# Optimization experiments

Hardware: AMD Instinct MI355X
Metric: run time of the kernel (lower is better)

## Reference

```python
import jax, jax.numpy as jnp
import numpy as np

B = 32; IMG = 224; P = 16; D = 768; NH = 12; HD = 64; L = 12; MLP = 3072; S0 = 197
NE = 10; LP = 40; NPL = 5; NC = 100; EPS = 1e-6
POS_PROMPT = (0, 1, 2, 3, 4)


def setup_inputs() -> dict:
    ks = jax.random.split(jax.random.key(0), 18)
    n = lambda k, shp: jax.random.normal(k, shp, jnp.float32) * 0.02
    return {
        "inputs": jax.random.normal(ks[0], (B, 3, IMG, IMG), jnp.float32),
        "expert_ids": jax.random.randint(ks[1], (B,), 0, NE),
        "patch_w": n(ks[2], (D, 3, P, P)),
        "patch_b": n(ks[3], (D,)),
        "cls_token": n(ks[4], (1, 1, D)),
        "pos_embed": n(ks[5], (1, S0, D)),
        "ln1_s": jnp.ones((L, D), jnp.float32),
        "ln1_b": jnp.zeros((L, D), jnp.float32),
        "qkv_w": n(ks[6], (L, D, 3 * D)),
        "qkv_b": n(ks[7], (L, 3 * D)),
        "proj_w": n(ks[8], (L, D, D)),
        "proj_b": n(ks[9], (L, D)),
        "ln2_s": jnp.ones((L, D), jnp.float32),
        "ln2_b": jnp.zeros((L, D), jnp.float32),
        "fc1_w": n(ks[10], (L, D, MLP)),
        "fc1_b": n(ks[11], (L, MLP)),
        "fc2_w": n(ks[12], (L, MLP, D)),
        "fc2_b": n(ks[13], (L, D)),
        "norm_s": jnp.ones((D,), jnp.float32),
        "norm_b": jnp.zeros((D,), jnp.float32),
        "prompts": jax.random.uniform(ks[14], (NPL, NE, LP, D), jnp.float32),
        "head_w": n(ks[15], (NE, D, NC)),
        "head_b": n(ks[16], (NE, NC)),
    }


def _ln(x, s, b):
    m = x.mean(-1, keepdims=True)
    v = ((x - m) ** 2).mean(-1, keepdims=True)
    return (x - m) * jax.lax.rsqrt(v + EPS) * s + b


def _forward(inputs, expert_ids, patch_w, patch_b, cls_token, pos_embed,
             ln1_s, ln1_b, qkv_w, qkv_b, proj_w, proj_b, ln2_s, ln2_b,
             fc1_w, fc1_b, fc2_w, fc2_b, norm_s, norm_b, prompts, head_w, head_b):
    # patch embed: conv stride 16 -> [B, D, 14, 14] -> [B, 196, D]
    x = jax.lax.conv_general_dilated(inputs, patch_w, (P, P), 'VALID',
                                     dimension_numbers=('NCHW', 'OIHW', 'NCHW'))
    x = x.reshape(B, D, -1).transpose(0, 2, 1) + patch_b
    x = jnp.concatenate([jnp.broadcast_to(cls_token, (B, 1, D)), x], axis=1) + pos_embed
    # per-sample expert prompt gather: [B, NPL, LP, D], plus cls pos bias
    bp = jnp.take(prompts, expert_ids, axis=1).transpose(1, 0, 2, 3) + pos_embed[0, 0]
    scale = 1.0 / np.sqrt(HD)
    for i in range(L):
        if i in POS_PROMPT:
            x = jnp.concatenate([x, bp[:, POS_PROMPT.index(i)]], axis=1)
        S = x.shape[1]
        h = _ln(x, ln1_s[i], ln1_b[i])
        qkv = (h @ qkv_w[i] + qkv_b[i]).reshape(B, S, 3, NH, HD).transpose(2, 0, 3, 1, 4)
        q, k, v = qkv[0], qkv[1], qkv[2]
        att = jax.nn.softmax(jnp.einsum('bhqd,bhkd->bhqk', q, k) * scale, axis=-1)
        o = jnp.einsum('bhqk,bhkd->bhqd', att, v).transpose(0, 2, 1, 3).reshape(B, S, D)
        x = x + o @ proj_w[i] + proj_b[i]
        h = _ln(x, ln2_s[i], ln2_b[i])
        x = x + jax.nn.gelu(h @ fc1_w[i] + fc1_b[i], approximate=False) @ fc2_w[i] + fc2_b[i]
        x = x[:, :S0]  # drop prompt tokens after each block
    feat = _ln(x, norm_s, norm_b)[:, 0]
    # per-sample expert head dispatch: gathered-weight batched matvec
    return jnp.einsum('bd,bdc->bc', feat, head_w[expert_ids]) + head_b[expert_ids]


def reference(inputs, expert_ids, patch_w, patch_b, cls_token, pos_embed,
              ln1_s, ln1_b, qkv_w, qkv_b, proj_w, proj_b, ln2_s, ln2_b,
              fc1_w, fc1_b, fc2_w, fc2_b, norm_s, norm_b, prompts, head_w, head_b):
    return _forward(inputs, expert_ids, patch_w, patch_b, cls_token, pos_embed,
                    ln1_s, ln1_b, qkv_w, qkv_b, proj_w, proj_b, ln2_s, ln2_b,
                    fc1_w, fc1_b, fc2_w, fc2_b, norm_s, norm_b, prompts, head_w, head_b)
```

## Files before the change

### kernel.cpp

```cpp
#include <hip/hip_runtime.h>

typedef unsigned short ushort_t;
typedef __attribute__((ext_vector_type(8))) short short8;
typedef __attribute__((ext_vector_type(4))) float floatx4;

#define D_    768
#define SMAX  237
#define S0_   197
#define RPAD  7680
#define NHEAD 12
#define BATCH 32


__device__ __forceinline__ ushort_t f2bf(float f) {
  union { float f; unsigned u; } v; v.f = f;
  unsigned r = v.u + 0x7FFFu + ((v.u >> 16) & 1u);
  return (ushort_t)(r >> 16);
}
__device__ __forceinline__ float bf2f(ushort_t u) {
  union { unsigned u; float f; } v; v.u = ((unsigned)u) << 16; return v.f;
}
__device__ __forceinline__ void async16(const void* g, void* l) {
  __builtin_amdgcn_global_load_lds((const __attribute__((address_space(1))) void*)g,
                                   (__attribute__((address_space(3))) void*)l, 16, 0, 0);
}

__global__ __launch_bounds__(256) void patchify_kernel(
    const float* __restrict__ in, ushort_t* __restrict__ Xp) {
  int rowid = blockIdx.x;
  int b = rowid / 196, p = rowid - b * 196;
  int py = p / 14, px = p - py * 14;
  int tid = threadIdx.x;
#pragma unroll
  for (int t = 0; t < 3; ++t) {
    int k = tid + t * 256;
    int c = k >> 8, rem = k & 255, i = rem >> 4, j = rem & 15;
    float v = in[(((size_t)b * 3 + c) * 224 + py * 16 + i) * 224 + px * 16 + j];
    Xp[(size_t)rowid * 768 + k] = f2bf(v);
  }
}

__global__ void cvt_bf16_kernel(const float* __restrict__ src, ushort_t* __restrict__ dst, int n) {
  int i = blockIdx.x * 256 + threadIdx.x;
  if (i < n) dst[i] = f2bf(src[i]);
}

__global__ void cls_fill_kernel(const float* __restrict__ cls, const float* __restrict__ pos,
                                float* __restrict__ X) {
  int b = blockIdx.x, d = threadIdx.x;
  X[(size_t)b * 768 + d] = cls[d] + pos[d];
}

__global__ void prompt_fill_kernel(const float* __restrict__ prompts, const float* __restrict__ pos,
                                   const int* __restrict__ eid, float* __restrict__ X, int layer) {
  int id = blockIdx.x;
  int b = id / 40, p = id - b * 40;
  int e = eid[b];
  float v = prompts[(((size_t)layer * 10 + e) * 40 + p) * 768 + threadIdx.x] + pos[threadIdx.x];
  X[((size_t)(197 + p) * 32 + b) * 768 + threadIdx.x] = v;
}

__global__ __launch_bounds__(256) void transpose_wts_kernel(
    const float* __restrict__ qkvw, const float* __restrict__ projw,
    const float* __restrict__ fc1w, const float* __restrict__ fc2w,
    ushort_t* __restrict__ wq, ushort_t* __restrict__ wp,
    ushort_t* __restrict__ w1, ushort_t* __restrict__ w2) {
  int id = blockIdx.x;
  const float* src; ushort_t* dst; int K, N, t;
  if (id < 1728)      { src = qkvw; dst = wq; K = 768;  N = 2304; t = id; }
  else if (id < 2304) { src = projw; dst = wp; K = 768;  N = 768;  t = id - 1728; }
  else if (id < 4608) { src = fc1w; dst = w1; K = 768;  N = 3072; t = id - 2304; }
  else                { src = fc2w; dst = w2; K = 3072; N = 768;  t = id - 4608; }
  int ntn = N >> 5;
  int k0 = (t / ntn) * 32, n0 = (t % ntn) * 32;
  __shared__ float tile[32][33];
  int tx = threadIdx.x & 31, ty = threadIdx.x >> 5;
#pragma unroll
  for (int q = 0; q < 4; ++q) {
    int kk = q * 8 + ty;
    tile[kk][tx] = src[(size_t)(k0 + kk) * N + n0 + tx];
  }
  __syncthreads();
#pragma unroll
  for (int q = 0; q < 4; ++q) {
    int nn = q * 8 + ty;
    dst[(size_t)(n0 + nn) * K + k0 + tx] = f2bf(tile[tx][nn]);
  }
}

__global__ __launch_bounds__(256) void ln_kernel(
    const float* __restrict__ X, const float* __restrict__ s, const float* __restrict__ bt,
    ushort_t* __restrict__ H) {
  int row = blockIdx.x, tid = threadIdx.x;
  const float* xr = X + (size_t)row * 768;
  float v0 = xr[tid], v1 = xr[tid + 256], v2 = xr[tid + 512];
  float sum = v0 + v1 + v2;
  float sq = v0 * v0 + v1 * v1 + v2 * v2;
#pragma unroll
  for (int off = 32; off; off >>= 1) {
    sum += __shfl_down(sum, off, 64);
    sq  += __shfl_down(sq,  off, 64);
  }
  __shared__ float red[8];
  int wv = tid >> 6, ln = tid & 63;
  if (ln == 0) { red[wv] = sum; red[4 + wv] = sq; }
  __syncthreads();
  if (tid == 0) {
    red[0] = red[0] + red[1] + red[2] + red[3];
    red[4] = red[4] + red[5] + red[6] + red[7];
  }
  __syncthreads();
  float mean = red[0] * (1.f / 768.f);
  float var  = red[4] * (1.f / 768.f) - mean * mean;
  float rs = rsqrtf(var + 1e-6f);
  ushort_t* hr = H + (size_t)row * 768;
  hr[tid]       = f2bf((v0 - mean) * rs * s[tid]       + bt[tid]);
  hr[tid + 256] = f2bf((v1 - mean) * rs * s[tid + 256] + bt[tid + 256]);
  hr[tid + 512] = f2bf((v2 - mean) * rs * s[tid + 512] + bt[tid + 512]);
}

enum { EPI_BF16 = 0, EPI_GELU = 1, EPI_RESID = 2, EPI_PATCH = 3 };

template <int EPI>
__global__ __launch_bounds__(256) void gemm_kernel(
    const ushort_t* __restrict__ A, int lda,
    const ushort_t* __restrict__ BT, int ldb,
    const float* __restrict__ bias,
    float* __restrict__ XO, ushort_t* __restrict__ O,
    const float* __restrict__ pos,
    int N, int nx, int my, int Klen, int nt) {
  __shared__ ushort_t As[128 * 32];
  __shared__ ushort_t Bs[128 * 32];
  int per = gridDim.x >> 3;
  int F = blockIdx.x;
  int T = (F & 7) * per + (F >> 3);
  if (T >= nt) return;
  int n_i = T % nx, rest = T / nx;
  int m_i = rest % my, kz = rest / my;
  int m0 = m_i * 128, n0 = n_i * 128;
  int kb = kz * Klen, ke = kb + Klen;

  int tid = threadIdx.x, lane = tid & 63, wv = tid >> 6;
  int wm = (wv >> 1) * 64, wn = (wv & 1) * 64;
  int fr = lane & 15, kg = lane >> 4;
  int sw = (kg ^ ((fr >> 1) & 3)) * 8;

  floatx4 acc[4][4];
#pragma unroll
  for (int i = 0; i < 4; ++i)
#pragma unroll
    for (int j = 0; j < 4; ++j) acc[i][j] = (floatx4){0.f, 0.f, 0.f, 0.f};

  for (int k0 = kb; k0 < ke; k0 += 32) {
#pragma unroll
    for (int t = 0; t < 2; ++t) {
      int flat = (wv * 2 + t) * 64 + lane;
      int row = flat >> 2;
      int ch = ((flat & 3) ^ ((flat >> 3) & 3)) * 8;
      async16(A + (size_t)(m0 + row) * lda + k0 + ch, &As[(wv * 2 + t) * 512]);
      async16(BT + (size_t)(n0 + row) * ldb + k0 + ch, &Bs[(wv * 2 + t) * 512]);
    }
    __syncthreads();
    short8 af[4], bfr[4];
#pragma unroll
    for (int i = 0; i < 4; ++i) af[i] = *(const short8*)&As[(wm + i * 16 + fr) * 32 + sw];
#pragma unroll
    for (int j = 0; j < 4; ++j) bfr[j] = *(const short8*)&Bs[(wn + j * 16 + fr) * 32 + sw];
#pragma unroll
    for (int i = 0; i < 4; ++i)
#pragma unroll
      for (int j = 0; j < 4; ++j)
        acc[i][j] = __builtin_amdgcn_mfma_f32_16x16x32_bf16(af[i], bfr[j], acc[i][j], 0, 0, 0);
    __syncthreads();
  }

  int rbase = (lane >> 4) * 4;
#pragma unroll
  for (int i = 0; i < 4; ++i) {
#pragma unroll
    for (int j = 0; j < 4; ++j) {
      int col = n0 + wn + j * 16 + fr;
#pragma unroll
      for (int r = 0; r < 4; ++r) {
        int row = m0 + wm + i * 16 + rbase + r;
        if (EPI == EPI_BF16) {
          O[(size_t)row * N + col] = f2bf(acc[i][j][r] + bias[col]);
        } else if (EPI == EPI_GELU) {
          float v = acc[i][j][r] + bias[col];
          float g = 0.5f * v * (1.0f + erff(v * 0.70710678118f));
          O[(size_t)row * N + col] = f2bf(g);
        } else if (EPI == EPI_RESID) {
          float v = acc[i][j][r] + (kz == 0 ? bias[col] : 0.f);
          atomicAdd(&XO[(size_t)row * 768 + col], v);
        } else {
          int b = row / 196, p = row - b * 196;
          size_t orow = (size_t)(1 + p) * 32 + b;
          XO[orow * 768 + col] = acc[i][j][r] + bias[col] + pos[(size_t)(1 + p) * 768 + col];
        }
      }
    }
  }
}

__global__ __launch_bounds__(256) void attn_kernel(ushort_t* __restrict__ qkv, int S) {
  __shared__ ushort_t Kc[64 * 64];
  __shared__ ushort_t Vt[64 * 72];
  __shared__ ushort_t Pb[4][16 * 72];
  int id = blockIdx.x;
  int qc = id & 3, bh = id >> 2;
  int b = bh / NHEAD, h = bh - b * NHEAD;
  int tid = threadIdx.x, lane = tid & 63, wv = tid >> 6;
  int fr = lane & 15, kg = lane >> 4;
  int q0 = qc * 64 + wv * 16;

  int qr = q0 + fr; if (qr > S - 1) qr = S - 1;
  const ushort_t* qp = qkv + ((size_t)qr * 32 + b) * 2304 + h * 64 + kg * 8;
  short8 qf0 = *(const short8*)qp;
  short8 qf1 = *(const short8*)(qp + 32);

  floatx4 oacc[4];
#pragma unroll
  for (int j = 0; j < 4; ++j) oacc[j] = (floatx4){0.f, 0.f, 0.f, 0.f};
  float lsum[4] = {0.f, 0.f, 0.f, 0.f};

  int ksw = kg ^ (fr & 7);
  int kst_g = (lane & 7) ^ ((lane >> 3) & 7);

  for (int c = 0; c < 4; ++c) {
    int key0 = c * 64;
    __syncthreads();
#pragma unroll
    for (int t = 0; t < 2; ++t) {
      int f = (wv * 2 + t) * 64 + lane;
      int kr = key0 + (f >> 3); if (kr > S - 1) kr = S - 1;
      async16(qkv + ((size_t)kr * 32 + b) * 2304 + 768 + h * 64 + kst_g * 8,
              &Kc[(wv * 2 + t) * 512]);
    }
#pragma unroll
    for (int t = 0; t < 2; ++t) {
      int kc = wv * 2 + t;
      int vr = key0 + lane; if (vr > S - 1) vr = S - 1;
      short8 vv = *(const short8*)(qkv + ((size_t)vr * 32 + b) * 2304 + 1536 + h * 64 + kc * 8);
#pragma unroll
      for (int e = 0; e < 8; ++e) Vt[(kc * 8 + e) * 72 + lane] = (ushort_t)vv[e];
    }
    __syncthreads();

    floatx4 sacc[4];
#pragma unroll
    for (int j = 0; j < 4; ++j) sacc[j] = (floatx4){0.f, 0.f, 0.f, 0.f};
#pragma unroll
    for (int j = 0; j < 4; ++j) {
      int krow = j * 16 + fr;
      short8 b0 = *(const short8*)&Kc[krow * 64 + ksw * 8];
      short8 b1 = *(const short8*)&Kc[krow * 64 + (ksw ^ 4) * 8];
      sacc[j] = __builtin_amdgcn_mfma_f32_16x16x32_bf16(qf0, b0, sacc[j], 0, 0, 0);
      sacc[j] = __builtin_amdgcn_mfma_f32_16x16x32_bf16(qf1, b1, sacc[j], 0, 0, 0);
    }

#pragma unroll
    for (int j = 0; j < 4; ++j) {
      int key = key0 + j * 16 + fr;
      bool valid = key < S;
#pragma unroll
      for (int r = 0; r < 4; ++r) {
        float e = valid ? __expf(sacc[j][r] * 0.125f) : 0.f;
        lsum[r] += e;
        Pb[wv][(kg * 4 + r) * 72 + j * 16 + fr] = f2bf(e);
      }
    }
    __syncthreads();

    const ushort_t* pp = &Pb[wv][fr * 72 + kg * 8];
    short8 p0 = *(const short8*)pp;
    short8 p1 = *(const short8*)(pp + 32);
#pragma unroll
    for (int j = 0; j < 4; ++j) {
      const ushort_t* vp = &Vt[(j * 16 + fr) * 72 + kg * 8];
      short8 v0 = *(const short8*)vp;
      short8 v1 = *(const short8*)(vp + 32);
      oacc[j] = __builtin_amdgcn_mfma_f32_16x16x32_bf16(p0, v0, oacc[j], 0, 0, 0);
      oacc[j] = __builtin_amdgcn_mfma_f32_16x16x32_bf16(p1, v1, oacc[j], 0, 0, 0);
    }
  }

#pragma unroll
  for (int r = 0; r < 4; ++r) {
#pragma unroll
    for (int m = 1; m <= 8; m <<= 1) lsum[r] += __shfl_xor(lsum[r], m, 64);
  }
#pragma unroll
  for (int r = 0; r < 4; ++r) {
    int q = q0 + kg * 4 + r;
    if (q < S) {
      float inv = 1.f / lsum[r];
      ushort_t* op = qkv + ((size_t)q * 32 + b) * 2304 + h * 64;
#pragma unroll
      for (int j = 0; j < 4; ++j) op[j * 16 + fr] = f2bf(oacc[j][r] * inv);
    }
  }
}

__global__ __launch_bounds__(256) void head_kernel(
    const float* __restrict__ X, const float* __restrict__ ns, const float* __restrict__ nb,
    const int* __restrict__ eid, const float* __restrict__ hw, const float* __restrict__ hb,
    float* __restrict__ out) {
  int b = blockIdx.x, tid = threadIdx.x;
  const float* xr = X + (size_t)b * 768;
  float v0 = xr[tid], v1 = xr[tid + 256], v2 = xr[tid + 512];
  float sum = v0 + v1 + v2;
  float sq = v0 * v0 + v1 * v1 + v2 * v2;
#pragma unroll
  for (int off = 32; off; off >>= 1) {
    sum += __shfl_down(sum, off, 64);
    sq  += __shfl_down(sq,  off, 64);
  }
  __shared__ float red[8];
  __shared__ float feat[768];
  int wv = tid >> 6, ln = tid & 63;
  if (ln == 0) { red[wv] = sum; red[4 + wv] = sq; }
  __syncthreads();
  if (tid == 0) {
    red[0] = red[0] + red[1] + red[2] + red[3];
    red[4] = red[4] + red[5] + red[6] + red[7];
  }
  __syncthreads();
  float mean = red[0] * (1.f / 768.f);
  float var  = red[4] * (1.f / 768.f) - mean * mean;
  float rs = rsqrtf(var + 1e-6f);
  feat[tid]       = (v0 - mean) * rs * ns[tid]       + nb[tid];
  feat[tid + 256] = (v1 - mean) * rs * ns[tid + 256] + nb[tid + 256];
  feat[tid + 512] = (v2 - mean) * rs * ns[tid + 512] + nb[tid + 512];
  __syncthreads();
  int e = eid[b];
  if (tid < 100) {
    float a = hb[e * 100 + tid];
    const float* w = hw + (size_t)e * 768 * 100 + tid;
#pragma unroll 4
    for (int d = 0; d < 768; ++d) a += feat[d] * w[(size_t)d * 100];
    out[b * 100 + tid] = a;
  }
}

extern "C" void kernel_launch(void* const* d_in, const int* in_sizes, int n_in,
                              void* d_out, int out_size, void* d_ws, size_t ws_size,
                              hipStream_t stream) {
  const float* inputs     = (const float*)d_in[0];
  const int*   expert_ids = (const int*)d_in[1];
  const float* patch_w    = (const float*)d_in[2];
  const float* patch_b    = (const float*)d_in[3];
  const float* cls_token  = (const float*)d_in[4];
  const float* pos_embed  = (const float*)d_in[5];
  const float* ln1_s      = (const float*)d_in[6];
  const float* ln1_b      = (const float*)d_in[7];
  const float* qkv_w      = (const float*)d_in[8];
  const float* qkv_b      = (const float*)d_in[9];
  const float* proj_w     = (const float*)d_in[10];
  const float* proj_b     = (const float*)d_in[11];
  const float* ln2_s      = (const float*)d_in[12];
  const float* ln2_b      = (const float*)d_in[13];
  const float* fc1_w      = (const float*)d_in[14];
  const float* fc1_b      = (const float*)d_in[15];
  const float* fc2_w      = (const float*)d_in[16];
  const float* fc2_b      = (const float*)d_in[17];
  const float* norm_s     = (const float*)d_in[18];
  const float* norm_b     = (const float*)d_in[19];
  const float* prompts    = (const float*)d_in[20];
  const float* head_w     = (const float*)d_in[21];
  const float* head_b     = (const float*)d_in[22];
  float* out = (float*)d_out;

  char* ws = (char*)d_ws;
  size_t off = 0;
  ushort_t* WTp = (ushort_t*)(ws + off); off += (size_t)768 * 768 * 2;
  ushort_t* WQ  = (ushort_t*)(ws + off); off += (size_t)2304 * 768 * 2;
  ushort_t* WP  = (ushort_t*)(ws + off); off += (size_t)768 * 768 * 2;
  ushort_t* W1  = (ushort_t*)(ws + off); off += (size_t)3072 * 768 * 2;
  ushort_t* W2  = (ushort_t*)(ws + off); off += (size_t)768 * 3072 * 2;
  float*    X   = (float*)(ws + off);    off += (size_t)RPAD * 768 * 4;
  ushort_t* H   = (ushort_t*)(ws + off); off += (size_t)RPAD * 768 * 2;
  ushort_t* QKV = (ushort_t*)(ws + off); off += (size_t)RPAD * 2304 * 2;
  ushort_t* MID = (ushort_t*)(ws + off); off += (size_t)RPAD * 3072 * 2;
  ushort_t* XP  = MID;

  cvt_bf16_kernel<<<(768 * 768 + 255) / 256, 256, 0, stream>>>(patch_w, WTp, 768 * 768);
  patchify_kernel<<<6272, 256, 0, stream>>>(inputs, XP);
  {
    int nt = 6 * 49, ntp = ((nt + 7) / 8) * 8;
    gemm_kernel<EPI_PATCH><<<ntp, 256, 0, stream>>>(
        XP, 768, WTp, 768, patch_b, X, nullptr, pos_embed, 768, 6, 49, 768, nt);
  }
  cls_fill_kernel<<<BATCH, 768, 0, stream>>>(cls_token, pos_embed, X);

  for (int i = 0; i < 12; ++i) {
    int S = (i < 5) ? SMAX : S0_;
    int MT = (i < 5) ? 60 : 50;
    if (i < 5)
      prompt_fill_kernel<<<BATCH * 40, 768, 0, stream>>>(prompts, pos_embed, expert_ids, X, i);
    transpose_wts_kernel<<<6912, 256, 0, stream>>>(
        qkv_w + (size_t)i * 768 * 2304, proj_w + (size_t)i * 768 * 768,
        fc1_w + (size_t)i * 768 * 3072, fc2_w + (size_t)i * 3072 * 768,
        WQ, WP, W1, W2);
    ln_kernel<<<MT * 128, 256, 0, stream>>>(X, ln1_s + i * 768, ln1_b + i * 768, H);
    {
      int nt = 18 * MT;
      gemm_kernel<EPI_BF16><<<nt, 256, 0, stream>>>(
          H, 768, WQ, 768, qkv_b + i * 2304, nullptr, QKV, nullptr, 2304, 18, MT, 768, nt);
    }
    attn_kernel<<<BATCH * NHEAD * 4, 256, 0, stream>>>(QKV, S);
    {
      int nt = 6 * MT * 2;
      gemm_kernel<EPI_RESID><<<nt, 256, 0, stream>>>(
          QKV, 2304, WP, 768, proj_b + i * 768, X, nullptr, nullptr, 768, 6, MT, 384, nt);
    }
    ln_kernel<<<MT * 128, 256, 0, stream>>>(X, ln2_s + i * 768, ln2_b + i * 768, H);
    {
      int nt = 24 * MT;
      gemm_kernel<EPI_GELU><<<nt, 256, 0, stream>>>(
          H, 768, W1, 768, fc1_b + i * 3072, nullptr, MID, nullptr, 3072, 24, MT, 768, nt);
    }
    {
      int nt = 6 * MT * 2;
      gemm_kernel<EPI_RESID><<<nt, 256, 0, stream>>>(
          MID, 3072, W2, 3072, fc2_b + i * 768, X, nullptr, nullptr, 768, 6, MT, 1536, nt);
    }
  }

  head_kernel<<<BATCH, 256, 0, stream>>>(X, norm_s, norm_b, expert_ids, head_w, head_b, out);
}
```

Before: 3.834 ms.

## Replace split-K atomics with 64-row GEMM tiles and hoist weight conversion

Adds a gemm64 kernel with 64x128 tiles for the N=768 projections, replacing split-K with atomicAdd by plain read-modify-write residual stores. All 12 layers' weights are transposed and converted to bf16 in one up-front launch when the workspace is large enough, instead of one launch per layer. The tile-swizzled 1D grid is dropped in favour of a plain 2D grid, which changes L2 locality. These changes trade atomic traffic and per-layer launches for a larger workspace and a different grid order.

```diff
diff --git a/kernel.cpp b/kernel.cpp
--- a/kernel.cpp
+++ b/kernel.cpp
@@ -64,13 +64,17 @@
     const float* __restrict__ qkvw, const float* __restrict__ projw,
     const float* __restrict__ fc1w, const float* __restrict__ fc2w,
     ushort_t* __restrict__ wq, ushort_t* __restrict__ wp,
-    ushort_t* __restrict__ w1, ushort_t* __restrict__ w2) {
+    ushort_t* __restrict__ w1, ushort_t* __restrict__ w2,
+    int l0, int slot_mul) {
   int id = blockIdx.x;
-  const float* src; ushort_t* dst; int K, N, t;
-  if (id < 1728)      { src = qkvw; dst = wq; K = 768;  N = 2304; t = id; }
-  else if (id < 2304) { src = projw; dst = wp; K = 768;  N = 768;  t = id - 1728; }
-  else if (id < 4608) { src = fc1w; dst = w1; K = 768;  N = 3072; t = id - 2304; }
-  else                { src = fc2w; dst = w2; K = 3072; N = 768;  t = id - 4608; }
+  int l = l0 + id / 6912;
+  int t = id % 6912;
+  size_t s = (size_t)(l * slot_mul);
+  const float* src; ushort_t* dst; int K, N;
+  if (t < 1728)      { src = qkvw + (size_t)l * 768 * 2304; dst = wq + s * 2304 * 768; K = 768;  N = 2304; }
+  else if (t < 2304) { src = projw + (size_t)l * 768 * 768;  dst = wp + s * 768 * 768;  K = 768;  N = 768;  t -= 1728; }
+  else if (t < 4608) { src = fc1w + (size_t)l * 768 * 3072;  dst = w1 + s * 768 * 3072; K = 768;  N = 3072; t -= 2304; }
+  else               { src = fc2w + (size_t)l * 3072 * 768;  dst = w2 + s * 3072 * 768; K = 3072; N = 768;  t -= 4608; }
   int ntn = N >> 5;
   int k0 = (t / ntn) * 32, n0 = (t % ntn) * 32;
   __shared__ float tile[32][33];
@@ -122,24 +126,35 @@
 enum { EPI_BF16 = 0, EPI_GELU = 1, EPI_RESID = 2, EPI_PATCH = 3 };
 
 template <int EPI>
+__device__ __forceinline__ void epi_store(float accv, int row, int col,
+                                          const float* bias, float* XO, ushort_t* O,
+                                          const float* pos, int N) {
+  if (EPI == EPI_BF16) {
+    O[(size_t)row * N + col] = f2bf(accv + bias[col]);
+  } else if (EPI == EPI_GELU) {
+    float v = accv + bias[col];
+    float g = 0.5f * v * (1.0f + erff(v * 0.70710678118f));
+    O[(size_t)row * N + col] = f2bf(g);
+  } else if (EPI == EPI_RESID) {
+    XO[(size_t)row * 768 + col] += accv + bias[col];
+  } else {
+    int b = row / 196, p = row - b * 196;
+    size_t orow = (size_t)(1 + p) * 32 + b;
+    XO[orow * 768 + col] = accv + bias[col] + pos[(size_t)(1 + p) * 768 + col];
+  }
+}
+
+template <int EPI>
 __global__ __launch_bounds__(256) void gemm_kernel(
     const ushort_t* __restrict__ A, int lda,
-    const ushort_t* __restrict__ BT, int ldb,
+    const ushort_t* __restrict__ BT,
     const float* __restrict__ bias,
     float* __restrict__ XO, ushort_t* __restrict__ O,
     const float* __restrict__ pos,
-    int N, int nx, int my, int Klen, int nt) {
+    int N, int K) {
   __shared__ ushort_t As[128 * 32];
   __shared__ ushort_t Bs[128 * 32];
-  int per = gridDim.x >> 3;
-  int F = blockIdx.x;
-  int T = (F & 7) * per + (F >> 3);
-  if (T >= nt) return;
-  int n_i = T % nx, rest = T / nx;
-  int m_i = rest % my, kz = rest / my;
-  int m0 = m_i * 128, n0 = n_i * 128;
-  int kb = kz * Klen, ke = kb + Klen;
-
+  int m0 = blockIdx.y * 128, n0 = blockIdx.x * 128;
   int tid = threadIdx.x, lane = tid & 63, wv = tid >> 6;
   int wm = (wv >> 1) * 64, wn = (wv & 1) * 64;
   int fr = lane & 15, kg = lane >> 4;
@@ -151,14 +166,14 @@
 #pragma unroll
     for (int j = 0; j < 4; ++j) acc[i][j] = (floatx4){0.f, 0.f, 0.f, 0.f};
 
-  for (int k0 = kb; k0 < ke; k0 += 32) {
+  for (int k0 = 0; k0 < K; k0 += 32) {
 #pragma unroll
     for (int t = 0; t < 2; ++t) {
       int flat = (wv * 2 + t) * 64 + lane;
       int row = flat >> 2;
       int ch = ((flat & 3) ^ ((flat >> 3) & 3)) * 8;
       async16(A + (size_t)(m0 + row) * lda + k0 + ch, &As[(wv * 2 + t) * 512]);
-      async16(BT + (size_t)(n0 + row) * ldb + k0 + ch, &Bs[(wv * 2 + t) * 512]);
+      async16(BT + (size_t)(n0 + row) * K + k0 + ch, &Bs[(wv * 2 + t) * 512]);
     }
     __syncthreads();
     short8 af[4], bfr[4];
@@ -176,30 +191,76 @@
 
   int rbase = (lane >> 4) * 4;
 #pragma unroll
-  for (int i = 0; i < 4; ++i) {
+  for (int i = 0; i < 4; ++i)
 #pragma unroll
     for (int j = 0; j < 4; ++j) {
       int col = n0 + wn + j * 16 + fr;
 #pragma unroll
-      for (int r = 0; r < 4; ++r) {
-        int row = m0 + wm + i * 16 + rbase + r;
-        if (EPI == EPI_BF16) {
-          O[(size_t)row * N + col] = f2bf(acc[i][j][r] + bias[col]);
-        } else if (EPI == EPI_GELU) {
-          float v = acc[i][j][r] + bias[col];
-          float g = 0.5f * v * (1.0f + erff(v * 0.70710678118f));
-          O[(size_t)row * N + col] = f2bf(g);
-        } else if (EPI == EPI_RESID) {
-          float v = acc[i][j][r] + (kz == 0 ? bias[col] : 0.f);
-          atomicAdd(&XO[(size_t)row * 768 + col], v);
-        } else {
-          int b = row / 196, p = row - b * 196;
-          size_t orow = (size_t)(1 + p) * 32 + b;
-          XO[orow * 768 + col] = acc[i][j][r] + bias[col] + pos[(size_t)(1 + p) * 768 + col];
-        }
-      }
-    }
-  }
+      for (int r = 0; r < 4; ++r)
+        epi_store<EPI>(acc[i][j][r], m0 + wm + i * 16 + rbase + r, col, bias, XO, O, pos, N);
+    }
+}
+
+template <int EPI>
+__global__ __launch_bounds__(256) void gemm64_kernel(
+    const ushort_t* __restrict__ A, int lda,
+    const ushort_t* __restrict__ BT,
+    const float* __restrict__ bias,
+    float* __restrict__ XO, ushort_t* __restrict__ O,
+    const float* __restrict__ pos,
+    int N, int K) {
+  __shared__ ushort_t As[64 * 32];
+  __shared__ ushort_t Bs[128 * 32];
+  int m0 = blockIdx.y * 64, n0 = blockIdx.x * 128;
+  int tid = threadIdx.x, lane = tid & 63, wv = tid >> 6;
+  int wm = (wv >> 1) * 32, wn = (wv & 1) * 64;
+  int fr = lane & 15, kg = lane >> 4;
+  int sw = (kg ^ ((fr >> 1) & 3)) * 8;
+
+  floatx4 acc[2][4];
+#pragma unroll
+  for (int i = 0; i < 2; ++i)
+#pragma unroll
+    for (int j = 0; j < 4; ++j) acc[i][j] = (floatx4){0.f, 0.f, 0.f, 0.f};
+
+  for (int k0 = 0; k0 < K; k0 += 32) {
+    {
+      int flat = wv * 64 + lane;
+      int row = flat >> 2;
+      int ch = ((flat & 3) ^ ((flat >> 3) & 3)) * 8;
+      async16(A + (size_t)(m0 + row) * lda + k0 + ch, &As[wv * 512]);
+    }
+#pragma unroll
+    for (int t = 0; t < 2; ++t) {
+      int flat = (wv * 2 + t) * 64 + lane;
+      int row = flat >> 2;
+      int ch = ((flat & 3) ^ ((flat >> 3) & 3)) * 8;
+      async16(BT + (size_t)(n0 + row) * K + k0 + ch, &Bs[(wv * 2 + t) * 512]);
+    }
+    __syncthreads();
+    short8 af[2], bfr[4];
+#pragma unroll
+    for (int i = 0; i < 2; ++i) af[i] = *(const short8*)&As[(wm + i * 16 + fr) * 32 + sw];
+#pragma unroll
+    for (int j = 0; j < 4; ++j) bfr[j] = *(const short8*)&Bs[(wn + j * 16 + fr) * 32 + sw];
+#pragma unroll
+    for (int i = 0; i < 2; ++i)
+#pragma unroll
+      for (int j = 0; j < 4; ++j)
+        acc[i][j] = __builtin_amdgcn_mfma_f32_16x16x32_bf16(af[i], bfr[j], acc[i][j], 0, 0, 0);
+    __syncthreads();
+  }
+
+  int rbase = (lane >> 4) * 4;
+#pragma unroll
+  for (int i = 0; i < 2; ++i)
+#pragma unroll
+    for (int j = 0; j < 4; ++j) {
+      int col = n0 + wn + j * 16 + fr;
+#pragma unroll
+      for (int r = 0; r < 4; ++r)
+        epi_store<EPI>(acc[i][j][r], m0 + wm + i * 16 + rbase + r, col, bias, XO, O, pos, N);
+    }
 }
 
 __global__ __launch_bounds__(256) void attn_kernel(ushort_t* __restrict__ qkv, int S) {
@@ -370,13 +431,17 @@
   const float* head_b     = (const float*)d_in[22];
   float* out = (float*)d_out;
 
+  const size_t kHoistNeed = 289100000ull;
+  bool hoist = ws_size >= kHoistNeed;
+  size_t slots = hoist ? 12 : 1;
+
   char* ws = (char*)d_ws;
   size_t off = 0;
   ushort_t* WTp = (ushort_t*)(ws + off); off += (size_t)768 * 768 * 2;
-  ushort_t* WQ  = (ushort_t*)(ws + off); off += (size_t)2304 * 768 * 2;
-  ushort_t* WP  = (ushort_t*)(ws + off); off += (size_t)768 * 768 * 2;
-  ushort_t* W1  = (ushort_t*)(ws + off); off += (size_t)3072 * 768 * 2;
-  ushort_t* W2  = (ushort_t*)(ws + off); off += (size_t)768 * 3072 * 2;
+  ushort_t* WQ  = (ushort_t*)(ws + off); off += slots * 2304 * 768 * 2;
+  ushort_t* WP  = (ushort_t*)(ws + off); off += slots * 768 * 768 * 2;
+  ushort_t* W1  = (ushort_t*)(ws + off); off += slots * 768 * 3072 * 2;
+  ushort_t* W2  = (ushort_t*)(ws + off); off += slots * 3072 * 768 * 2;
   float*    X   = (float*)(ws + off);    off += (size_t)RPAD * 768 * 4;
   ushort_t* H   = (ushort_t*)(ws + off); off += (size_t)RPAD * 768 * 2;
   ushort_t* QKV = (ushort_t*)(ws + off); off += (size_t)RPAD * 2304 * 2;
@@ -385,45 +450,38 @@
 
   cvt_bf16_kernel<<<(768 * 768 + 255) / 256, 256, 0, stream>>>(patch_w, WTp, 768 * 768);
   patchify_kernel<<<6272, 256, 0, stream>>>(inputs, XP);
-  {
-    int nt = 6 * 49, ntp = ((nt + 7) / 8) * 8;
-    gemm_kernel<EPI_PATCH><<<ntp, 256, 0, stream>>>(
-        XP, 768, WTp, 768, patch_b, X, nullptr, pos_embed, 768, 6, 49, 768, nt);
-  }
+  gemm64_kernel<EPI_PATCH><<<dim3(6, 98), 256, 0, stream>>>(
+      XP, 768, WTp, patch_b, X, nullptr, pos_embed, 768, 768);
   cls_fill_kernel<<<BATCH, 768, 0, stream>>>(cls_token, pos_embed, X);
+
+  if (hoist)
+    transpose_wts_kernel<<<6912 * 12, 256, 0, stream>>>(
+        qkv_w, proj_w, fc1_w, fc2_w, WQ, WP, W1, W2, 0, 1);
 
   for (int i = 0; i < 12; ++i) {
     int S = (i < 5) ? SMAX : S0_;
     int MT = (i < 5) ? 60 : 50;
     if (i < 5)
       prompt_fill_kernel<<<BATCH * 40, 768, 0, stream>>>(prompts, pos_embed, expert_ids, X, i);
-    transpose_wts_kernel<<<6912, 256, 0, stream>>>(
-        qkv_w + (size_t)i * 768 * 2304, proj_w + (size_t)i * 768 * 768,
-        fc1_w + (size_t)i * 768 * 3072, fc2_w + (size_t)i * 3072 * 768,
-        WQ, WP, W1, W2);
+    if (!hoist)
+      transpose_wts_kernel<<<6912, 256, 0, stream>>>(
+          qkv_w, proj_w, fc1_w, fc2_w, WQ, WP, W1, W2, i, 0);
+    ushort_t* WQi = WQ + (hoist ? (size_t)i * 2304 * 768 : 0);
+    ushort_t* WPi = WP + (hoist ? (size_t)i * 768 * 768 : 0);
+    ushort_t* W1i = W1 + (hoist ? (size_t)i * 768 * 3072 : 0);
+    ushort_t* W2i = W2 + (hoist ? (size_t)i * 3072 * 768 : 0);
+
     ln_kernel<<<MT * 128, 256, 0, stream>>>(X, ln1_s + i * 768, ln1_b + i * 768, H);
-    {
-      int nt = 18 * MT;
-      gemm_kernel<EPI_BF16><<<nt, 256, 0, stream>>>(
-          H, 768, WQ, 768, qkv_b + i * 2304, nullptr, QKV, nullptr, 2304, 18, MT, 768, nt);
-    }
+    gemm_kernel<EPI_BF16><<<dim3(18, MT), 256, 0, stream>>>(
+        H, 768, WQi, qkv_b + i * 2304, nullptr, QKV, nullptr, 2304, 768);
     attn_kernel<<<BATCH * NHEAD * 4, 256, 0, stream>>>(QKV, S);
-    {
-      int nt = 6 * MT * 2;
-      gemm_kernel<EPI_RESID><<<nt, 256, 0, stream>>>(
-          QKV, 2304, WP, 768, proj_b + i * 768, X, nullptr, nullptr, 768, 6, MT, 384, nt);
-    }
+    gemm64_kernel<EPI_RESID><<<dim3(6, MT * 2), 256, 0, stream>>>(
+        QKV, 2304, WPi, proj_b + i * 768, X, nullptr, nullptr, 768, 768);
     ln_kernel<<<MT * 128, 256, 0, stream>>>(X, ln2_s + i * 768, ln2_b + i * 768, H);
-    {
-      int nt = 24 * MT;
-      gemm_kernel<EPI_GELU><<<nt, 256, 0, stream>>>(
-          H, 768, W1, 768, fc1_b + i * 3072, nullptr, MID, nullptr, 3072, 24, MT, 768, nt);
-    }
-    {
-      int nt = 6 * MT * 2;
-      gemm_kernel<EPI_RESID><<<nt, 256, 0, stream>>>(
-          MID, 3072, W2, 3072, fc2_b + i * 768, X, nullptr, nullptr, 768, 6, MT, 1536, nt);
-    }
+    gemm_kernel<EPI_GELU><<<dim3(24, MT), 256, 0, stream>>>(
+        H, 768, W1i, fc1_b + i * 3072, nullptr, MID, nullptr, 3072, 768);
+    gemm64_kernel<EPI_RESID><<<dim3(6, MT * 2), 256, 0, stream>>>(
+        MID, 3072, W2i, fc2_b + i * 768, X, nullptr, nullptr, 768, 3072);
   }
 
   head_kernel<<<BATCH, 256, 0, stream>>>(X, norm_s, norm_b, expert_ids, head_w, head_b, out);
```

Result: faster. 3.484 ms (-9.1%).
